# Kernel tuning notes

Measured on AMD Instinct MI355X. Metric: run time of the kernel, lower is better.

## Reference

```python
import jax, jax.numpy as jnp
import numpy as np

N = 50000      # nodes
E = 800000     # edges (avg degree 16)
F = 128        # num_features
H = 128        # hidden_channels
C = 16         # num_classes
KEEP = 0.5     # dropout keep prob


def setup_inputs() -> dict:
    key = jax.random.key(0)
    ks = jax.random.split(key, 7)
    x = jax.random.normal(ks[0], (N, F), dtype=jnp.float32)
    edge_index = jax.random.randint(ks[1], (2, E), 0, N, dtype=jnp.int64)
    W1 = jax.random.normal(ks[2], (F, H), dtype=jnp.float32) / np.float32(np.sqrt(F))
    b1 = jnp.zeros((H,), dtype=jnp.float32)
    W2 = jax.random.normal(ks[3], (H, C), dtype=jnp.float32) / np.float32(np.sqrt(H))
    b2 = jnp.zeros((C,), dtype=jnp.float32)
    # deterministic dropout mask (train-mode dropout, prob=0.5), pre-scaled by 1/keep
    dropout_mask = (jax.random.uniform(ks[4], (N, H)) < KEEP).astype(jnp.float32) / np.float32(KEEP)
    return {"x": x, "edge_index": edge_index, "W1": W1, "b1": b1,
            "W2": W2, "b2": b2, "dropout_mask": dropout_mask}


def _gather_mean(h, src, dst, n_nodes):
    # irregular gather (h[src]) + segment scatter-add at dst, then mean by in-degree
    agg = jax.ops.segment_sum(h[src], dst, num_segments=n_nodes)  # [N, c]
    deg = jax.ops.segment_sum(jnp.ones_like(dst, dtype=h.dtype), dst, num_segments=n_nodes)
    return agg / jnp.maximum(deg, 1.0)[:, None]


def reference(x, edge_index, W1, b1, W2, b2, dropout_mask):
    src, dst = edge_index[0], edge_index[1]
    # linmaps1: 0th->1st order broadcast; identity for singleton reference domains
    h = _gather_mean(x, src, dst, N)          # ConvolutionalLayer_1P #1: gather
    h = h @ W1 + b1                           # linear transform
    h = jax.nn.relu(h)
    h = h * dropout_mask                      # Dropout(prob=0.5)
    h = _gather_mean(h, src, dst, N)          # ConvolutionalLayer_1P #2: gather
    out = h @ W2 + b2
    # linmaps0: 1st->0th order reduce; identity for singleton domains
    return out
```

## Files before the change

### kernel.cpp

```cpp
#include <hip/hip_runtime.h>

#define NNODES 50000
#define NEDGES 800000
#define FDIM 128
#define HDIM 128
#define CDIM 16

#define NBUCK 256
#define BCAP 6144
#define NBA 391
#define NMB 782

typedef __attribute__((ext_vector_type(8))) short bf16x8;
typedef __attribute__((ext_vector_type(4))) float f32x4;

__device__ __forceinline__ ushort f32_to_bf16_rne(float f) {
  unsigned u = __float_as_uint(f);
  unsigned rounded = u + 0x7fffu + ((u >> 16) & 1u);
  return (ushort)(rounded >> 16);
}
__device__ __forceinline__ float bf_lo(unsigned u) { return __uint_as_float(u << 16); }
__device__ __forceinline__ float bf_hi(unsigned u) { return __uint_as_float(u & 0xffff0000u); }

__global__ __launch_bounds__(256) void k_binA(
    const int* __restrict__ src, const int* __restrict__ dst,
    int* __restrict__ gcur, unsigned* __restrict__ ebuf,
    const float* __restrict__ mask, unsigned* __restrict__ maskb) {
  __shared__ int cnt[NBUCK];
  __shared__ int base[NBUCK];
  int tid = threadIdx.x;
  if (blockIdx.x < NBA) {
    int e0 = blockIdx.x * 2048;
    cnt[tid] = 0;
    __syncthreads();
    int sv[8], dv[8];
    #pragma unroll
    for (int i = 0; i < 8; ++i) {
      int e = e0 + i * 256 + tid;
      if (e < NEDGES) {
        sv[i] = src[e];
        dv[i] = dst[e];
        atomicAdd(&cnt[dv[i] >> 8], 1);
      } else {
        dv[i] = -1;
      }
    }
    __syncthreads();
    base[tid] = atomicAdd(&gcur[tid], cnt[tid]);
    cnt[tid] = 0;
    __syncthreads();
    #pragma unroll
    for (int i = 0; i < 8; ++i) {
      if (dv[i] >= 0) {
        int b = dv[i] >> 8;
        int pos = base[b] + atomicAdd(&cnt[b], 1);
        if (pos < BCAP)
          ebuf[b * BCAP + pos] = ((unsigned)(dv[i] & 255) << 16) | (unsigned)sv[i];
      }
    }
    return;
  }
  int t = (blockIdx.x - NBA) * 256 + tid;
  if (t < 200000) {
    const float* mp = mask + (size_t)t * 32;
    unsigned bits = 0;
    #pragma unroll
    for (int i = 0; i < 8; ++i) {
      float4 m = *reinterpret_cast<const float4*>(mp + i * 4);
      bits |= (m.x != 0.f ? 1u : 0u) << (i * 4 + 0);
      bits |= (m.y != 0.f ? 1u : 0u) << (i * 4 + 1);
      bits |= (m.z != 0.f ? 1u : 0u) << (i * 4 + 2);
      bits |= (m.w != 0.f ? 1u : 0u) << (i * 4 + 3);
    }
    maskb[t] = bits;
  }
}

__global__ __launch_bounds__(256) void k_binB_cast(
    const int* __restrict__ gcur, const unsigned* __restrict__ ebuf,
    int* __restrict__ deg, int* __restrict__ offs, ushort* __restrict__ ssrc,
    const float* __restrict__ x, ushort* __restrict__ xh,
    const float* __restrict__ W1, ushort* __restrict__ W1T,
    const float* __restrict__ W2, ushort* __restrict__ W2T) {
  __shared__ int s[NBUCK];
  __shared__ int doff[NBUCK];
  __shared__ int dcur[NBUCK];
  int tid = threadIdx.x;
  if (blockIdx.x < NBUCK) {
    int b = blockIdx.x;
    int c = gcur[tid];
    if (c > BCAP) c = BCAP;
    s[tid] = c;
    for (int off = 1; off < 256; off <<= 1) {
      __syncthreads();
      int t = (tid >= off) ? s[tid - off] : 0;
      __syncthreads();
      s[tid] += t;
    }
    __syncthreads();
    int my_base = (b > 0) ? s[b - 1] : 0;
    int count = s[b] - my_base;

    dcur[tid] = 0;
    __syncthreads();
    const unsigned* eb = &ebuf[b * BCAP];
    for (int e = tid; e < count; e += 256) {
      atomicAdd(&dcur[eb[e] >> 16], 1);
    }
    __syncthreads();
    int dn = dcur[tid];
    s[tid] = dn;
    for (int off = 1; off < 256; off <<= 1) {
      __syncthreads();
      int t = (tid >= off) ? s[tid - off] : 0;
      __syncthreads();
      s[tid] += t;
    }
    __syncthreads();
    doff[tid] = s[tid] - dn;
    int node = b * 256 + tid;
    if (node < NNODES) {
      deg[node] = dn;
      offs[node] = my_base + doff[tid];
    }
    dcur[tid] = 0;
    __syncthreads();

    for (int e = tid; e < count; e += 256) {
      unsigned v = eb[e];
      int loc = v >> 16;
      int pos = my_base + doff[loc] + atomicAdd(&dcur[loc], 1);
      ssrc[pos] = (ushort)(v & 0xffffu);
    }
    return;
  }
  int t = (blockIdx.x - NBUCK) * 256 + tid;
  if (t < 1600000) {
    float4 v = *reinterpret_cast<const float4*>(&x[t * 4]);
    ushort4 o;
    o.x = f32_to_bf16_rne(v.x);
    o.y = f32_to_bf16_rne(v.y);
    o.z = f32_to_bf16_rne(v.z);
    o.w = f32_to_bf16_rne(v.w);
    *reinterpret_cast<ushort4*>(&xh[t * 4]) = o;
    return;
  }
  t -= 1600000;
  if (t < 16384) {
    int c = t >> 7, k = t & 127;
    W1T[c * 128 + k] = f32_to_bf16_rne(W1[k * 128 + c]);
    return;
  }
  t -= 16384;
  if (t < 2048) {
    int c = t >> 7, k = t & 127;
    W2T[c * 128 + k] = f32_to_bf16_rne(W2[k * 16 + c]);
  }
}

__global__ __launch_bounds__(256) void k_spmm1(
    const ushort* __restrict__ xh, const int* __restrict__ offs,
    const int* __restrict__ deg, const ushort* __restrict__ ssrc,
    ushort* __restrict__ aggh) {
  int tid = threadIdx.x;
  int grp = tid >> 4;
  int l16 = tid & 15;
  int n = blockIdx.x * 16 + grp;
  if (n >= NNODES) return;
  int start = offs[n];
  int d = deg[n];
  const ushort* base = xh + l16 * 8;
  float a0[8] = {0,0,0,0,0,0,0,0};
  float a1[8] = {0,0,0,0,0,0,0,0};
  float a2[8] = {0,0,0,0,0,0,0,0};
  float a3[8] = {0,0,0,0,0,0,0,0};
  int j = 0;
  for (; j + 3 < d; j += 4) {
    int s0 = ssrc[start + j + 0];
    int s1 = ssrc[start + j + 1];
    int s2 = ssrc[start + j + 2];
    int s3 = ssrc[start + j + 3];
    uint4 u0 = *reinterpret_cast<const uint4*>(base + s0 * FDIM);
    uint4 u1 = *reinterpret_cast<const uint4*>(base + s1 * FDIM);
    uint4 u2 = *reinterpret_cast<const uint4*>(base + s2 * FDIM);
    uint4 u3 = *reinterpret_cast<const uint4*>(base + s3 * FDIM);
    a0[0] += bf_lo(u0.x); a0[1] += bf_hi(u0.x); a0[2] += bf_lo(u0.y); a0[3] += bf_hi(u0.y);
    a0[4] += bf_lo(u0.z); a0[5] += bf_hi(u0.z); a0[6] += bf_lo(u0.w); a0[7] += bf_hi(u0.w);
    a1[0] += bf_lo(u1.x); a1[1] += bf_hi(u1.x); a1[2] += bf_lo(u1.y); a1[3] += bf_hi(u1.y);
    a1[4] += bf_lo(u1.z); a1[5] += bf_hi(u1.z); a1[6] += bf_lo(u1.w); a1[7] += bf_hi(u1.w);
    a2[0] += bf_lo(u2.x); a2[1] += bf_hi(u2.x); a2[2] += bf_lo(u2.y); a2[3] += bf_hi(u2.y);
    a2[4] += bf_lo(u2.z); a2[5] += bf_hi(u2.z); a2[6] += bf_lo(u2.w); a2[7] += bf_hi(u2.w);
    a3[0] += bf_lo(u3.x); a3[1] += bf_hi(u3.x); a3[2] += bf_lo(u3.y); a3[3] += bf_hi(u3.y);
    a3[4] += bf_lo(u3.z); a3[5] += bf_hi(u3.z); a3[6] += bf_lo(u3.w); a3[7] += bf_hi(u3.w);
  }
  for (; j < d; ++j) {
    int s0 = ssrc[start + j];
    uint4 u0 = *reinterpret_cast<const uint4*>(base + s0 * FDIM);
    a0[0] += bf_lo(u0.x); a0[1] += bf_hi(u0.x); a0[2] += bf_lo(u0.y); a0[3] += bf_hi(u0.y);
    a0[4] += bf_lo(u0.z); a0[5] += bf_hi(u0.z); a0[6] += bf_lo(u0.w); a0[7] += bf_hi(u0.w);
  }
  float inv = 1.0f / (float)(d > 0 ? d : 1);
  unsigned r[4];
  #pragma unroll
  for (int k = 0; k < 4; ++k) {
    float e0 = (a0[2 * k] + a1[2 * k] + a2[2 * k] + a3[2 * k]) * inv;
    float e1 = (a0[2 * k + 1] + a1[2 * k + 1] + a2[2 * k + 1] + a3[2 * k + 1]) * inv;
    r[k] = (unsigned)f32_to_bf16_rne(e0) | ((unsigned)f32_to_bf16_rne(e1) << 16);
  }
  uint4 o; o.x = r[0]; o.y = r[1]; o.z = r[2]; o.w = r[3];
  *reinterpret_cast<uint4*>(&aggh[(size_t)n * FDIM + l16 * 8]) = o;
}

#define HT_STRIDE 132
__global__ __launch_bounds__(256) void k_dense(
    const ushort* __restrict__ aggh, const ushort* __restrict__ W1T,
    const float* __restrict__ b1, const unsigned* __restrict__ maskb,
    const ushort* __restrict__ W2T, ushort* __restrict__ zh) {
  __shared__ ushort hT[4][16 * HT_STRIDE];
  int w = threadIdx.x >> 6;
  int lane = threadIdx.x & 63;
  int nw = blockIdx.x * 64 + w * 16;
  if (nw >= NNODES) return;
  int l15 = lane & 15, quad = lane >> 4;

  f32x4 acc[8];
  #pragma unroll
  for (int ct = 0; ct < 8; ++ct) acc[ct] = (f32x4){0.f, 0.f, 0.f, 0.f};

  uint4 mb[4];
  #pragma unroll
  for (int r = 0; r < 4; ++r) {
    mb[r] = *reinterpret_cast<const uint4*>(&maskb[(size_t)(nw + quad * 4 + r) * 4]);
  }

  const ushort* arow = &aggh[(size_t)(nw + l15) * 128 + quad * 8];
  #pragma unroll
  for (int kk = 0; kk < 4; ++kk) {
    bf16x8 a = *reinterpret_cast<const bf16x8*>(arow + kk * 32);
    #pragma unroll
    for (int ct = 0; ct < 8; ++ct) {
      bf16x8 b = *reinterpret_cast<const bf16x8*>(
          &W1T[(size_t)(ct * 16 + l15) * 128 + kk * 32 + quad * 8]);
      acc[ct] = __builtin_amdgcn_mfma_f32_16x16x32_bf16(a, b, acc[ct], 0, 0, 0);
    }
  }

  ushort* ht = hT[w];
  #pragma unroll
  for (int ct = 0; ct < 8; ++ct) {
    int col = ct * 16 + l15;
    float bb = b1[col];
    int shift = (ct & 1) * 16 + l15;
    #pragma unroll
    for (int r = 0; r < 4; ++r) {
      unsigned word = (ct & 2) ? ((ct & 4) ? mb[r].w : mb[r].y)
                               : ((ct & 4) ? mb[r].z : mb[r].x);
      float v = acc[ct][r] + bb;
      v = v > 0.f ? v : 0.f;
      v = ((word >> shift) & 1u) ? (v + v) : 0.f;
      ht[(quad * 4 + r) * HT_STRIDE + col] = f32_to_bf16_rne(v);
    }
  }

  f32x4 zacc = (f32x4){0.f, 0.f, 0.f, 0.f};
  #pragma unroll
  for (int kk = 0; kk < 4; ++kk) {
    const ushort* ap = &ht[l15 * HT_STRIDE + kk * 32 + quad * 8];
    ushort4 alo = *reinterpret_cast<const ushort4*>(ap);
    ushort4 ahi = *reinterpret_cast<const ushort4*>(ap + 4);
    bf16x8 a2 = (bf16x8){(short)alo.x, (short)alo.y, (short)alo.z, (short)alo.w,
                         (short)ahi.x, (short)ahi.y, (short)ahi.z, (short)ahi.w};
    bf16x8 b2 = *reinterpret_cast<const bf16x8*>(&W2T[l15 * 128 + kk * 32 + quad * 8]);
    zacc = __builtin_amdgcn_mfma_f32_16x16x32_bf16(a2, b2, zacc, 0, 0, 0);
  }
  #pragma unroll
  for (int r = 0; r < 4; ++r) {
    zh[(size_t)(nw + quad * 4 + r) * 16 + l15] = f32_to_bf16_rne(zacc[r]);
  }
}

__global__ __launch_bounds__(256) void k_spmm2(
    const ushort* __restrict__ zh, const int* __restrict__ offs,
    const int* __restrict__ deg, const ushort* __restrict__ ssrc,
    const float* __restrict__ b2, float* __restrict__ out) {
  int tid = threadIdx.x;
  int nl = tid >> 3, c2 = tid & 7;
  int n = blockIdx.x * 32 + nl;
  if (n >= NNODES) return;
  int start = offs[n], d = deg[n];
  const ushort* zb = zh + c2 * 2;
  float a0 = 0.f, a1 = 0.f, b0 = 0.f, b1v = 0.f;
  float c0 = 0.f, c1 = 0.f, d0 = 0.f, d1 = 0.f;
  int j = 0;
  for (; j + 7 < d; j += 8) {
    int s0 = ssrc[start + j + 0], s1 = ssrc[start + j + 1];
    int s2 = ssrc[start + j + 2], s3 = ssrc[start + j + 3];
    int s4 = ssrc[start + j + 4], s5 = ssrc[start + j + 5];
    int s6 = ssrc[start + j + 6], s7 = ssrc[start + j + 7];
    unsigned u0 = *reinterpret_cast<const unsigned*>(zb + s0 * 16);
    unsigned u1 = *reinterpret_cast<const unsigned*>(zb + s1 * 16);
    unsigned u2 = *reinterpret_cast<const unsigned*>(zb + s2 * 16);
    unsigned u3 = *reinterpret_cast<const unsigned*>(zb + s3 * 16);
    unsigned u4 = *reinterpret_cast<const unsigned*>(zb + s4 * 16);
    unsigned u5 = *reinterpret_cast<const unsigned*>(zb + s5 * 16);
    unsigned u6 = *reinterpret_cast<const unsigned*>(zb + s6 * 16);
    unsigned u7 = *reinterpret_cast<const unsigned*>(zb + s7 * 16);
    a0 += bf_lo(u0); a1 += bf_hi(u0);
    b0 += bf_lo(u1); b1v += bf_hi(u1);
    c0 += bf_lo(u2); c1 += bf_hi(u2);
    d0 += bf_lo(u3); d1 += bf_hi(u3);
    a0 += bf_lo(u4); a1 += bf_hi(u4);
    b0 += bf_lo(u5); b1v += bf_hi(u5);
    c0 += bf_lo(u6); c1 += bf_hi(u6);
    d0 += bf_lo(u7); d1 += bf_hi(u7);
  }
  for (; j < d; ++j) {
    int s0 = ssrc[start + j];
    unsigned u0 = *reinterpret_cast<const unsigned*>(zb + s0 * 16);
    a0 += bf_lo(u0); a1 += bf_hi(u0);
  }
  float inv = 1.0f / (float)(d > 0 ? d : 1);
  float o0 = ((a0 + b0) + (c0 + d0)) * inv + b2[c2 * 2 + 0];
  float o1 = ((a1 + b1v) + (c1 + d1)) * inv + b2[c2 * 2 + 1];
  float2 o; o.x = o0; o.y = o1;
  *reinterpret_cast<float2*>(&out[(size_t)n * 16 + c2 * 2]) = o;
}


extern "C" void kernel_launch(void* const* d_in, const int* in_sizes, int n_in,
                              void* d_out, int out_size, void* d_ws, size_t ws_size,
                              hipStream_t stream) {
  const float* x    = (const float*)d_in[0];
  const int*   ei   = (const int*)d_in[1];
  const float* W1   = (const float*)d_in[2];
  const float* b1   = (const float*)d_in[3];
  const float* W2   = (const float*)d_in[4];
  const float* b2   = (const float*)d_in[5];
  const float* mask = (const float*)d_in[6];
  float* out = (float*)d_out;

  const int* src = ei;
  const int* dst = ei + NEDGES;

  char* ws = (char*)d_ws;
  size_t o = 0;
  auto alloc = [&](size_t bytes) -> void* {
    void* p = ws + o;
    o += (bytes + 255) & ~(size_t)255;
    return p;
  };
  ushort*   aggh  = (ushort*)alloc((size_t)NNODES * 128 * 2);
  ushort*   xh    = (ushort*)alloc((size_t)NNODES * 128 * 2);
  ushort*   zh    = (ushort*)alloc((size_t)NNODES * 16 * 2);
  ushort*   W1T   = (ushort*)alloc((size_t)128 * 128 * 2);
  ushort*   W2T   = (ushort*)alloc((size_t)16 * 128 * 2);
  int*      deg   = (int*)alloc((size_t)NNODES * 4);
  int*      offs  = (int*)alloc((size_t)NNODES * 4);
  int*      gcur  = (int*)alloc((size_t)NBUCK * 4);
  unsigned* ebuf  = (unsigned*)alloc((size_t)NBUCK * BCAP * 4);
  ushort*   ssrc  = (ushort*)alloc((size_t)NEDGES * 2);
  unsigned* maskb = (unsigned*)alloc((size_t)NNODES * 4 * 4);

  int cast_blocks = (1600000 + 16384 + 2048 + 255) / 256;

  hipMemsetAsync(gcur, 0, NBUCK * sizeof(int), stream);
  k_binA<<<NBA + NMB, 256, 0, stream>>>(src, dst, gcur, ebuf, mask, maskb);
  k_binB_cast<<<NBUCK + cast_blocks, 256, 0, stream>>>(gcur, ebuf, deg, offs, ssrc,
                                                       x, xh, W1, W1T, W2, W2T);
  k_spmm1<<<(NNODES + 15) / 16, 256, 0, stream>>>(xh, offs, deg, ssrc, aggh);
  k_dense<<<(NNODES + 63) / 64, 256, 0, stream>>>(aggh, W1T, b1, maskb, W2T, zh);
  k_spmm2<<<(NNODES + 31) / 32, 256, 0, stream>>>(zh, offs, deg, ssrc, b2, out);
}
```

Before: 181.8 us.

## Fuse first neighbor gather into dense MFMA kernel, dropping aggregated intermediate

Merges the first SpMM gather with the dense MLP kernel. Each lane gathers the neighbor rows directly into its MFMA A-fragment layout (node per lane m, 32-element k-slices per quad) and feeds them straight to the W1 MFMAs. This removes the aggh write and re-read and one kernel launch. The cost is that each lane now walks its own node's edge list serially with four 16-byte loads per edge, so lanes with different degrees diverge. The work is also spread over fewer threads, which reduces memory-level parallelism compared with the old 16-lanes-per-node gather.

```diff
diff --git a/kernel.cpp b/kernel.cpp
--- a/kernel.cpp
+++ b/kernel.cpp
@@ -158,99 +158,100 @@
   }
 }
 
-__global__ __launch_bounds__(256) void k_spmm1(
+#define ACCQ(A, U) do { \
+    A[0] += bf_lo(U.x); A[1] += bf_hi(U.x); \
+    A[2] += bf_lo(U.y); A[3] += bf_hi(U.y); \
+    A[4] += bf_lo(U.z); A[5] += bf_hi(U.z); \
+    A[6] += bf_lo(U.w); A[7] += bf_hi(U.w); } while (0)
+
+#define HT_STRIDE 132
+__global__ __launch_bounds__(256) void k_gather_dense(
     const ushort* __restrict__ xh, const int* __restrict__ offs,
     const int* __restrict__ deg, const ushort* __restrict__ ssrc,
-    ushort* __restrict__ aggh) {
-  int tid = threadIdx.x;
-  int grp = tid >> 4;
-  int l16 = tid & 15;
-  int n = blockIdx.x * 16 + grp;
-  if (n >= NNODES) return;
-  int start = offs[n];
-  int d = deg[n];
-  const ushort* base = xh + l16 * 8;
+    const ushort* __restrict__ W1T, const float* __restrict__ b1,
+    const unsigned* __restrict__ maskb, const ushort* __restrict__ W2T,
+    ushort* __restrict__ zh) {
+  __shared__ ushort hT[4][16 * HT_STRIDE];
+  int w = threadIdx.x >> 6;
+  int lane = threadIdx.x & 63;
+  int m = lane & 15, quad = lane >> 4;
+  int nw = blockIdx.x * 64 + w * 16;
+  int n = nw + m;
+  int start = 0, d = 0;
+  if (n < NNODES) { start = offs[n]; d = deg[n]; }
+
   float a0[8] = {0,0,0,0,0,0,0,0};
   float a1[8] = {0,0,0,0,0,0,0,0};
   float a2[8] = {0,0,0,0,0,0,0,0};
   float a3[8] = {0,0,0,0,0,0,0,0};
+  const ushort* xb = xh + quad * 8;
   int j = 0;
-  for (; j + 3 < d; j += 4) {
-    int s0 = ssrc[start + j + 0];
+  for (; j + 1 < d; j += 2) {
+    int s0 = ssrc[start + j];
     int s1 = ssrc[start + j + 1];
-    int s2 = ssrc[start + j + 2];
-    int s3 = ssrc[start + j + 3];
-    uint4 u0 = *reinterpret_cast<const uint4*>(base + s0 * FDIM);
-    uint4 u1 = *reinterpret_cast<const uint4*>(base + s1 * FDIM);
-    uint4 u2 = *reinterpret_cast<const uint4*>(base + s2 * FDIM);
-    uint4 u3 = *reinterpret_cast<const uint4*>(base + s3 * FDIM);
-    a0[0] += bf_lo(u0.x); a0[1] += bf_hi(u0.x); a0[2] += bf_lo(u0.y); a0[3] += bf_hi(u0.y);
-    a0[4] += bf_lo(u0.z); a0[5] += bf_hi(u0.z); a0[6] += bf_lo(u0.w); a0[7] += bf_hi(u0.w);
-    a1[0] += bf_lo(u1.x); a1[1] += bf_hi(u1.x); a1[2] += bf_lo(u1.y); a1[3] += bf_hi(u1.y);
-    a1[4] += bf_lo(u1.z); a1[5] += bf_hi(u1.z); a1[6] += bf_lo(u1.w); a1[7] += bf_hi(u1.w);
-    a2[0] += bf_lo(u2.x); a2[1] += bf_hi(u2.x); a2[2] += bf_lo(u2.y); a2[3] += bf_hi(u2.y);
-    a2[4] += bf_lo(u2.z); a2[5] += bf_hi(u2.z); a2[6] += bf_lo(u2.w); a2[7] += bf_hi(u2.w);
-    a3[0] += bf_lo(u3.x); a3[1] += bf_hi(u3.x); a3[2] += bf_lo(u3.y); a3[3] += bf_hi(u3.y);
-    a3[4] += bf_lo(u3.z); a3[5] += bf_hi(u3.z); a3[6] += bf_lo(u3.w); a3[7] += bf_hi(u3.w);
-  }
-  for (; j < d; ++j) {
+    const ushort* r0 = xb + s0 * FDIM;
+    const ushort* r1 = xb + s1 * FDIM;
+    uint4 u00 = *reinterpret_cast<const uint4*>(r0);
+    uint4 u01 = *reinterpret_cast<const uint4*>(r0 + 32);
+    uint4 u02 = *reinterpret_cast<const uint4*>(r0 + 64);
+    uint4 u03 = *reinterpret_cast<const uint4*>(r0 + 96);
+    uint4 u10 = *reinterpret_cast<const uint4*>(r1);
+    uint4 u11 = *reinterpret_cast<const uint4*>(r1 + 32);
+    uint4 u12 = *reinterpret_cast<const uint4*>(r1 + 64);
+    uint4 u13 = *reinterpret_cast<const uint4*>(r1 + 96);
+    ACCQ(a0, u00); ACCQ(a1, u01); ACCQ(a2, u02); ACCQ(a3, u03);
+    ACCQ(a0, u10); ACCQ(a1, u11); ACCQ(a2, u12); ACCQ(a3, u13);
+  }
+  if (j < d) {
     int s0 = ssrc[start + j];
-    uint4 u0 = *reinterpret_cast<const uint4*>(base + s0 * FDIM);
-    a0[0] += bf_lo(u0.x); a0[1] += bf_hi(u0.x); a0[2] += bf_lo(u0.y); a0[3] += bf_hi(u0.y);
-    a0[4] += bf_lo(u0.z); a0[5] += bf_hi(u0.z); a0[6] += bf_lo(u0.w); a0[7] += bf_hi(u0.w);
+    const ushort* r0 = xb + s0 * FDIM;
+    uint4 u00 = *reinterpret_cast<const uint4*>(r0);
+    uint4 u01 = *reinterpret_cast<const uint4*>(r0 + 32);
+    uint4 u02 = *reinterpret_cast<const uint4*>(r0 + 64);
+    uint4 u03 = *reinterpret_cast<const uint4*>(r0 + 96);
+    ACCQ(a0, u00); ACCQ(a1, u01); ACCQ(a2, u02); ACCQ(a3, u03);
   }
   float inv = 1.0f / (float)(d > 0 ? d : 1);
-  unsigned r[4];
-  #pragma unroll
-  for (int k = 0; k < 4; ++k) {
-    float e0 = (a0[2 * k] + a1[2 * k] + a2[2 * k] + a3[2 * k]) * inv;
-    float e1 = (a0[2 * k + 1] + a1[2 * k + 1] + a2[2 * k + 1] + a3[2 * k + 1]) * inv;
-    r[k] = (unsigned)f32_to_bf16_rne(e0) | ((unsigned)f32_to_bf16_rne(e1) << 16);
-  }
-  uint4 o; o.x = r[0]; o.y = r[1]; o.z = r[2]; o.w = r[3];
-  *reinterpret_cast<uint4*>(&aggh[(size_t)n * FDIM + l16 * 8]) = o;
-}
-
-#define HT_STRIDE 132
-__global__ __launch_bounds__(256) void k_dense(
-    const ushort* __restrict__ aggh, const ushort* __restrict__ W1T,
-    const float* __restrict__ b1, const unsigned* __restrict__ maskb,
-    const ushort* __restrict__ W2T, ushort* __restrict__ zh) {
-  __shared__ ushort hT[4][16 * HT_STRIDE];
-  int w = threadIdx.x >> 6;
-  int lane = threadIdx.x & 63;
-  int nw = blockIdx.x * 64 + w * 16;
-  if (nw >= NNODES) return;
-  int l15 = lane & 15, quad = lane >> 4;
+  #define PACK8(A) (bf16x8){ \
+      (short)f32_to_bf16_rne(A[0] * inv), (short)f32_to_bf16_rne(A[1] * inv), \
+      (short)f32_to_bf16_rne(A[2] * inv), (short)f32_to_bf16_rne(A[3] * inv), \
+      (short)f32_to_bf16_rne(A[4] * inv), (short)f32_to_bf16_rne(A[5] * inv), \
+      (short)f32_to_bf16_rne(A[6] * inv), (short)f32_to_bf16_rne(A[7] * inv)}
+  bf16x8 af0 = PACK8(a0);
+  bf16x8 af1 = PACK8(a1);
+  bf16x8 af2 = PACK8(a2);
+  bf16x8 af3 = PACK8(a3);
 
   f32x4 acc[8];
   #pragma unroll
   for (int ct = 0; ct < 8; ++ct) acc[ct] = (f32x4){0.f, 0.f, 0.f, 0.f};
+  #pragma unroll
+  for (int ct = 0; ct < 8; ++ct) {
+    const ushort* bp = &W1T[(size_t)(ct * 16 + m) * 128 + quad * 8];
+    acc[ct] = __builtin_amdgcn_mfma_f32_16x16x32_bf16(
+        af0, *reinterpret_cast<const bf16x8*>(bp), acc[ct], 0, 0, 0);
+    acc[ct] = __builtin_amdgcn_mfma_f32_16x16x32_bf16(
+        af1, *reinterpret_cast<const bf16x8*>(bp + 32), acc[ct], 0, 0, 0);
+    acc[ct] = __builtin_amdgcn_mfma_f32_16x16x32_bf16(
+        af2, *reinterpret_cast<const bf16x8*>(bp + 64), acc[ct], 0, 0, 0);
+    acc[ct] = __builtin_amdgcn_mfma_f32_16x16x32_bf16(
+        af3, *reinterpret_cast<const bf16x8*>(bp + 96), acc[ct], 0, 0, 0);
+  }
 
   uint4 mb[4];
   #pragma unroll
   for (int r = 0; r < 4; ++r) {
-    mb[r] = *reinterpret_cast<const uint4*>(&maskb[(size_t)(nw + quad * 4 + r) * 4]);
-  }
-
-  const ushort* arow = &aggh[(size_t)(nw + l15) * 128 + quad * 8];
-  #pragma unroll
-  for (int kk = 0; kk < 4; ++kk) {
-    bf16x8 a = *reinterpret_cast<const bf16x8*>(arow + kk * 32);
-    #pragma unroll
-    for (int ct = 0; ct < 8; ++ct) {
-      bf16x8 b = *reinterpret_cast<const bf16x8*>(
-          &W1T[(size_t)(ct * 16 + l15) * 128 + kk * 32 + quad * 8]);
-      acc[ct] = __builtin_amdgcn_mfma_f32_16x16x32_bf16(a, b, acc[ct], 0, 0, 0);
-    }
+    int nr = nw + quad * 4 + r;
+    if (nr >= NNODES) nr = NNODES - 1;
+    mb[r] = *reinterpret_cast<const uint4*>(&maskb[(size_t)nr * 4]);
   }
 
   ushort* ht = hT[w];
   #pragma unroll
   for (int ct = 0; ct < 8; ++ct) {
-    int col = ct * 16 + l15;
+    int col = ct * 16 + m;
     float bb = b1[col];
-    int shift = (ct & 1) * 16 + l15;
+    int shift = (ct & 1) * 16 + m;
     #pragma unroll
     for (int r = 0; r < 4; ++r) {
       unsigned word = (ct & 2) ? ((ct & 4) ? mb[r].w : mb[r].y)
@@ -265,17 +266,19 @@
   f32x4 zacc = (f32x4){0.f, 0.f, 0.f, 0.f};
   #pragma unroll
   for (int kk = 0; kk < 4; ++kk) {
-    const ushort* ap = &ht[l15 * HT_STRIDE + kk * 32 + quad * 8];
+    const ushort* ap = &ht[m * HT_STRIDE + kk * 32 + quad * 8];
     ushort4 alo = *reinterpret_cast<const ushort4*>(ap);
     ushort4 ahi = *reinterpret_cast<const ushort4*>(ap + 4);
-    bf16x8 a2 = (bf16x8){(short)alo.x, (short)alo.y, (short)alo.z, (short)alo.w,
-                         (short)ahi.x, (short)ahi.y, (short)ahi.z, (short)ahi.w};
-    bf16x8 b2 = *reinterpret_cast<const bf16x8*>(&W2T[l15 * 128 + kk * 32 + quad * 8]);
-    zacc = __builtin_amdgcn_mfma_f32_16x16x32_bf16(a2, b2, zacc, 0, 0, 0);
+    bf16x8 afr = (bf16x8){(short)alo.x, (short)alo.y, (short)alo.z, (short)alo.w,
+                          (short)ahi.x, (short)ahi.y, (short)ahi.z, (short)ahi.w};
+    bf16x8 b2 = *reinterpret_cast<const bf16x8*>(&W2T[m * 128 + kk * 32 + quad * 8]);
+    zacc = __builtin_amdgcn_mfma_f32_16x16x32_bf16(afr, b2, zacc, 0, 0, 0);
   }
   #pragma unroll
   for (int r = 0; r < 4; ++r) {
-    zh[(size_t)(nw + quad * 4 + r) * 16 + l15] = f32_to_bf16_rne(zacc[r]);
+    int node = nw + quad * 4 + r;
+    if (node < NNODES)
+      zh[(size_t)node * 16 + m] = f32_to_bf16_rne(zacc[r]);
   }
 }
 
@@ -349,7 +352,6 @@
     o += (bytes + 255) & ~(size_t)255;
     return p;
   };
-  ushort*   aggh  = (ushort*)alloc((size_t)NNODES * 128 * 2);
   ushort*   xh    = (ushort*)alloc((size_t)NNODES * 128 * 2);
   ushort*   zh    = (ushort*)alloc((size_t)NNODES * 16 * 2);
   ushort*   W1T   = (ushort*)alloc((size_t)128 * 128 * 2);
@@ -367,7 +369,7 @@
   k_binA<<<NBA + NMB, 256, 0, stream>>>(src, dst, gcur, ebuf, mask, maskb);
   k_binB_cast<<<NBUCK + cast_blocks, 256, 0, stream>>>(gcur, ebuf, deg, offs, ssrc,
                                                        x, xh, W1, W1T, W2, W2T);
-  k_spmm1<<<(NNODES + 15) / 16, 256, 0, stream>>>(xh, offs, deg, ssrc, aggh);
-  k_dense<<<(NNODES + 63) / 64, 256, 0, stream>>>(aggh, W1T, b1, maskb, W2T, zh);
+  k_gather_dense<<<(NNODES + 63) / 64, 256, 0, stream>>>(xh, offs, deg, ssrc,
+                                                         W1T, b1, maskb, W2T, zh);
   k_spmm2<<<(NNODES + 31) / 32, 256, 0, stream>>>(zh, offs, deg, ssrc, b2, out);
 }
```

Measured after the change: 188.6 us. 3.7% more time.

## Fuse first gather-mean SpMM with dense W1/ReLU/dropout/W2 stage via shared memory

Applied to the files above, without the earlier changes.

Merges the first neighbor aggregation kernel with the dense MLP kernel. Each block aggregates 16 nodes into shared memory, then splits the W1 MFMA output tiles across its four waves before one wave runs the W2 projection. This removes the aggh global round trip (a write and reread of N×128 bf16) and one kernel launch. In exchange it adds two block barriers, leaves three waves idle during the W2 step, and drops the bounds check, which relies on N being divisible by 16.

```diff
diff --git a/kernel.cpp b/kernel.cpp
--- a/kernel.cpp
+++ b/kernel.cpp
@@ -158,15 +158,20 @@
   }
 }
 
-__global__ __launch_bounds__(256) void k_spmm1(
+#define HT_STRIDE 132
+__global__ __launch_bounds__(256) void k_fused1(
     const ushort* __restrict__ xh, const int* __restrict__ offs,
     const int* __restrict__ deg, const ushort* __restrict__ ssrc,
-    ushort* __restrict__ aggh) {
+    const ushort* __restrict__ W1T, const float* __restrict__ b1,
+    const unsigned* __restrict__ maskb, const ushort* __restrict__ W2T,
+    ushort* __restrict__ zh) {
+  __shared__ ushort sh[16 * HT_STRIDE];
+  __shared__ ushort ht[16 * HT_STRIDE];
   int tid = threadIdx.x;
   int grp = tid >> 4;
   int l16 = tid & 15;
-  int n = blockIdx.x * 16 + grp;
-  if (n >= NNODES) return;
+  int nw = blockIdx.x * 16;
+  int n = nw + grp;
   int start = offs[n];
   int d = deg[n];
   const ushort* base = xh + l16 * 8;
@@ -207,75 +212,74 @@
     float e1 = (a0[2 * k + 1] + a1[2 * k + 1] + a2[2 * k + 1] + a3[2 * k + 1]) * inv;
     r[k] = (unsigned)f32_to_bf16_rne(e0) | ((unsigned)f32_to_bf16_rne(e1) << 16);
   }
-  uint4 o; o.x = r[0]; o.y = r[1]; o.z = r[2]; o.w = r[3];
-  *reinterpret_cast<uint4*>(&aggh[(size_t)n * FDIM + l16 * 8]) = o;
-}
-
-#define HT_STRIDE 132
-__global__ __launch_bounds__(256) void k_dense(
-    const ushort* __restrict__ aggh, const ushort* __restrict__ W1T,
-    const float* __restrict__ b1, const unsigned* __restrict__ maskb,
-    const ushort* __restrict__ W2T, ushort* __restrict__ zh) {
-  __shared__ ushort hT[4][16 * HT_STRIDE];
-  int w = threadIdx.x >> 6;
-  int lane = threadIdx.x & 63;
-  int nw = blockIdx.x * 64 + w * 16;
-  if (nw >= NNODES) return;
-  int l15 = lane & 15, quad = lane >> 4;
-
-  f32x4 acc[8];
-  #pragma unroll
-  for (int ct = 0; ct < 8; ++ct) acc[ct] = (f32x4){0.f, 0.f, 0.f, 0.f};
-
-  uint4 mb[4];
-  #pragma unroll
-  for (int r = 0; r < 4; ++r) {
-    mb[r] = *reinterpret_cast<const uint4*>(&maskb[(size_t)(nw + quad * 4 + r) * 4]);
-  }
-
-  const ushort* arow = &aggh[(size_t)(nw + l15) * 128 + quad * 8];
+  *reinterpret_cast<uint4*>(&sh[grp * HT_STRIDE + l16 * 8]) =
+      (uint4){r[0], r[1], r[2], r[3]};
+  __syncthreads();
+
+  int w = tid >> 6;
+  int lane = tid & 63;
+  int m = lane & 15, quad = lane >> 4;
+  int ct0 = 2 * w, ct1 = 2 * w + 1;
+
+  bf16x8 af[4];
   #pragma unroll
   for (int kk = 0; kk < 4; ++kk) {
-    bf16x8 a = *reinterpret_cast<const bf16x8*>(arow + kk * 32);
-    #pragma unroll
-    for (int ct = 0; ct < 8; ++ct) {
-      bf16x8 b = *reinterpret_cast<const bf16x8*>(
-          &W1T[(size_t)(ct * 16 + l15) * 128 + kk * 32 + quad * 8]);
-      acc[ct] = __builtin_amdgcn_mfma_f32_16x16x32_bf16(a, b, acc[ct], 0, 0, 0);
-    }
-  }
-
-  ushort* ht = hT[w];
-  #pragma unroll
-  for (int ct = 0; ct < 8; ++ct) {
-    int col = ct * 16 + l15;
-    float bb = b1[col];
-    int shift = (ct & 1) * 16 + l15;
-    #pragma unroll
-    for (int r = 0; r < 4; ++r) {
-      unsigned word = (ct & 2) ? ((ct & 4) ? mb[r].w : mb[r].y)
-                               : ((ct & 4) ? mb[r].z : mb[r].x);
-      float v = acc[ct][r] + bb;
-      v = v > 0.f ? v : 0.f;
-      v = ((word >> shift) & 1u) ? (v + v) : 0.f;
-      ht[(quad * 4 + r) * HT_STRIDE + col] = f32_to_bf16_rne(v);
-    }
-  }
-
-  f32x4 zacc = (f32x4){0.f, 0.f, 0.f, 0.f};
-  #pragma unroll
-  for (int kk = 0; kk < 4; ++kk) {
-    const ushort* ap = &ht[l15 * HT_STRIDE + kk * 32 + quad * 8];
+    const ushort* ap = &sh[m * HT_STRIDE + kk * 32 + quad * 8];
     ushort4 alo = *reinterpret_cast<const ushort4*>(ap);
     ushort4 ahi = *reinterpret_cast<const ushort4*>(ap + 4);
-    bf16x8 a2 = (bf16x8){(short)alo.x, (short)alo.y, (short)alo.z, (short)alo.w,
-                         (short)ahi.x, (short)ahi.y, (short)ahi.z, (short)ahi.w};
-    bf16x8 b2 = *reinterpret_cast<const bf16x8*>(&W2T[l15 * 128 + kk * 32 + quad * 8]);
-    zacc = __builtin_amdgcn_mfma_f32_16x16x32_bf16(a2, b2, zacc, 0, 0, 0);
-  }
-  #pragma unroll
-  for (int r = 0; r < 4; ++r) {
-    zh[(size_t)(nw + quad * 4 + r) * 16 + l15] = f32_to_bf16_rne(zacc[r]);
+    af[kk] = (bf16x8){(short)alo.x, (short)alo.y, (short)alo.z, (short)alo.w,
+                      (short)ahi.x, (short)ahi.y, (short)ahi.z, (short)ahi.w};
+  }
+  f32x4 acc0 = (f32x4){0.f, 0.f, 0.f, 0.f};
+  f32x4 acc1 = (f32x4){0.f, 0.f, 0.f, 0.f};
+  const ushort* bp0 = &W1T[(size_t)(ct0 * 16 + m) * 128 + quad * 8];
+  const ushort* bp1 = &W1T[(size_t)(ct1 * 16 + m) * 128 + quad * 8];
+  #pragma unroll
+  for (int kk = 0; kk < 4; ++kk) {
+    acc0 = __builtin_amdgcn_mfma_f32_16x16x32_bf16(
+        af[kk], *reinterpret_cast<const bf16x8*>(bp0 + kk * 32), acc0, 0, 0, 0);
+    acc1 = __builtin_amdgcn_mfma_f32_16x16x32_bf16(
+        af[kk], *reinterpret_cast<const bf16x8*>(bp1 + kk * 32), acc1, 0, 0, 0);
+  }
+
+  unsigned mbw[4];
+  #pragma unroll
+  for (int rr = 0; rr < 4; ++rr) {
+    mbw[rr] = maskb[(size_t)(nw + quad * 4 + rr) * 4 + w];
+  }
+  float bb0 = b1[ct0 * 16 + m];
+  float bb1 = b1[ct1 * 16 + m];
+  int sh0 = m;
+  int sh1 = 16 + m;
+  #pragma unroll
+  for (int rr = 0; rr < 4; ++rr) {
+    float v0 = acc0[rr] + bb0;
+    v0 = v0 > 0.f ? v0 : 0.f;
+    v0 = ((mbw[rr] >> sh0) & 1u) ? (v0 + v0) : 0.f;
+    ht[(quad * 4 + rr) * HT_STRIDE + ct0 * 16 + m] = f32_to_bf16_rne(v0);
+    float v1 = acc1[rr] + bb1;
+    v1 = v1 > 0.f ? v1 : 0.f;
+    v1 = ((mbw[rr] >> sh1) & 1u) ? (v1 + v1) : 0.f;
+    ht[(quad * 4 + rr) * HT_STRIDE + ct1 * 16 + m] = f32_to_bf16_rne(v1);
+  }
+  __syncthreads();
+
+  if (w == 0) {
+    f32x4 zacc = (f32x4){0.f, 0.f, 0.f, 0.f};
+    #pragma unroll
+    for (int kk = 0; kk < 4; ++kk) {
+      const ushort* ap = &ht[m * HT_STRIDE + kk * 32 + quad * 8];
+      ushort4 alo = *reinterpret_cast<const ushort4*>(ap);
+      ushort4 ahi = *reinterpret_cast<const ushort4*>(ap + 4);
+      bf16x8 afr = (bf16x8){(short)alo.x, (short)alo.y, (short)alo.z, (short)alo.w,
+                            (short)ahi.x, (short)ahi.y, (short)ahi.z, (short)ahi.w};
+      bf16x8 b2f = *reinterpret_cast<const bf16x8*>(&W2T[m * 128 + kk * 32 + quad * 8]);
+      zacc = __builtin_amdgcn_mfma_f32_16x16x32_bf16(afr, b2f, zacc, 0, 0, 0);
+    }
+    #pragma unroll
+    for (int rr = 0; rr < 4; ++rr) {
+      zh[(size_t)(nw + quad * 4 + rr) * 16 + m] = f32_to_bf16_rne(zacc[rr]);
+    }
   }
 }
 
@@ -349,7 +353,6 @@
     o += (bytes + 255) & ~(size_t)255;
     return p;
   };
-  ushort*   aggh  = (ushort*)alloc((size_t)NNODES * 128 * 2);
   ushort*   xh    = (ushort*)alloc((size_t)NNODES * 128 * 2);
   ushort*   zh    = (ushort*)alloc((size_t)NNODES * 16 * 2);
   ushort*   W1T   = (ushort*)alloc((size_t)128 * 128 * 2);
@@ -367,7 +370,7 @@
   k_binA<<<NBA + NMB, 256, 0, stream>>>(src, dst, gcur, ebuf, mask, maskb);
   k_binB_cast<<<NBUCK + cast_blocks, 256, 0, stream>>>(gcur, ebuf, deg, offs, ssrc,
                                                        x, xh, W1, W1T, W2, W2T);
-  k_spmm1<<<(NNODES + 15) / 16, 256, 0, stream>>>(xh, offs, deg, ssrc, aggh);
-  k_dense<<<(NNODES + 63) / 64, 256, 0, stream>>>(aggh, W1T, b1, maskb, W2T, zh);
+  k_fused1<<<NNODES / 16, 256, 0, stream>>>(xh, offs, deg, ssrc,
+                                            W1T, b1, maskb, W2T, zh);
   k_spmm2<<<(NNODES + 31) / 32, 256, 0, stream>>>(zh, offs, deg, ssrc, b2, out);
 }
```

New measurement: 172.2 us (median of 2 runs). 1.06x faster.

## Split xh into column quarters and map quarters to XCD pairs in spmm1

Applied to the files above, without the earlier changes.

The bf16 copy of x is stored as four column-quarter planes of 32 features each, and the first gather kernel assigns each quarter to a pair of XCDs through the block index. Each XCD's L2 then only has to hold a 3.2 MB slice of the feature table instead of the whole 12.8 MB table, which should raise gather cache hit rates. Each node's quarter is handled by 4 lanes with an 8-way unrolled loop and a single accumulator, and the output is written with nontemporal stores. The scheme relies on blocks being dispatched round-robin across 8 XCDs, and with only four lanes per row each row fetch is 64 bytes, so access granularity gets finer.

```diff
diff --git a/kernel.cpp b/kernel.cpp
--- a/kernel.cpp
+++ b/kernel.cpp
@@ -10,9 +10,12 @@
 #define BCAP 6144
 #define NBA 391
 #define NMB 782
+#define NQ 4
+#define NT1 782
 
 typedef __attribute__((ext_vector_type(8))) short bf16x8;
 typedef __attribute__((ext_vector_type(4))) float f32x4;
+typedef __attribute__((ext_vector_type(4))) unsigned u32x4;
 
 __device__ __forceinline__ ushort f32_to_bf16_rne(float f) {
   unsigned u = __float_as_uint(f);
@@ -142,7 +145,11 @@
     o.y = f32_to_bf16_rne(v.y);
     o.z = f32_to_bf16_rne(v.z);
     o.w = f32_to_bf16_rne(v.w);
-    *reinterpret_cast<ushort4*>(&xh[t * 4]) = o;
+    int e0 = t * 4;
+    int n = e0 >> 7;
+    int c = e0 & 127;
+    int idx = ((c >> 5) * NNODES + n) * 32 + (c & 31);
+    *reinterpret_cast<ushort4*>(&xh[idx]) = o;
     return;
   }
   t -= 1600000;
@@ -158,57 +165,64 @@
   }
 }
 
-__global__ __launch_bounds__(256) void k_spmm1(
+#define ACCA(A, U) do { \
+    A[0] += bf_lo(U.x); A[1] += bf_hi(U.x); \
+    A[2] += bf_lo(U.y); A[3] += bf_hi(U.y); \
+    A[4] += bf_lo(U.z); A[5] += bf_hi(U.z); \
+    A[6] += bf_lo(U.w); A[7] += bf_hi(U.w); } while (0)
+
+__global__ __launch_bounds__(256) void k_spmm1x(
     const ushort* __restrict__ xh, const int* __restrict__ offs,
     const int* __restrict__ deg, const ushort* __restrict__ ssrc,
     ushort* __restrict__ aggh) {
+  int b = blockIdx.x;
+  int xcd = b & 7;
+  int q = xcd >> 1;
+  int nb = (b >> 3) * 2 + (xcd & 1);
   int tid = threadIdx.x;
-  int grp = tid >> 4;
-  int l16 = tid & 15;
-  int n = blockIdx.x * 16 + grp;
+  int grp = tid >> 2;
+  int l4 = tid & 3;
+  int n = nb * 64 + grp;
   if (n >= NNODES) return;
   int start = offs[n];
   int d = deg[n];
-  const ushort* base = xh + l16 * 8;
-  float a0[8] = {0,0,0,0,0,0,0,0};
-  float a1[8] = {0,0,0,0,0,0,0,0};
-  float a2[8] = {0,0,0,0,0,0,0,0};
-  float a3[8] = {0,0,0,0,0,0,0,0};
+  const ushort* xq = xh + (size_t)q * NNODES * 32 + l4 * 8;
+  float acc[8] = {0, 0, 0, 0, 0, 0, 0, 0};
   int j = 0;
-  for (; j + 3 < d; j += 4) {
+  for (; j + 7 < d; j += 8) {
     int s0 = ssrc[start + j + 0];
     int s1 = ssrc[start + j + 1];
     int s2 = ssrc[start + j + 2];
     int s3 = ssrc[start + j + 3];
-    uint4 u0 = *reinterpret_cast<const uint4*>(base + s0 * FDIM);
-    uint4 u1 = *reinterpret_cast<const uint4*>(base + s1 * FDIM);
-    uint4 u2 = *reinterpret_cast<const uint4*>(base + s2 * FDIM);
-    uint4 u3 = *reinterpret_cast<const uint4*>(base + s3 * FDIM);
-    a0[0] += bf_lo(u0.x); a0[1] += bf_hi(u0.x); a0[2] += bf_lo(u0.y); a0[3] += bf_hi(u0.y);
-    a0[4] += bf_lo(u0.z); a0[5] += bf_hi(u0.z); a0[6] += bf_lo(u0.w); a0[7] += bf_hi(u0.w);
-    a1[0] += bf_lo(u1.x); a1[1] += bf_hi(u1.x); a1[2] += bf_lo(u1.y); a1[3] += bf_hi(u1.y);
-    a1[4] += bf_lo(u1.z); a1[5] += bf_hi(u1.z); a1[6] += bf_lo(u1.w); a1[7] += bf_hi(u1.w);
-    a2[0] += bf_lo(u2.x); a2[1] += bf_hi(u2.x); a2[2] += bf_lo(u2.y); a2[3] += bf_hi(u2.y);
-    a2[4] += bf_lo(u2.z); a2[5] += bf_hi(u2.z); a2[6] += bf_lo(u2.w); a2[7] += bf_hi(u2.w);
-    a3[0] += bf_lo(u3.x); a3[1] += bf_hi(u3.x); a3[2] += bf_lo(u3.y); a3[3] += bf_hi(u3.y);
-    a3[4] += bf_lo(u3.z); a3[5] += bf_hi(u3.z); a3[6] += bf_lo(u3.w); a3[7] += bf_hi(u3.w);
+    int s4 = ssrc[start + j + 4];
+    int s5 = ssrc[start + j + 5];
+    int s6 = ssrc[start + j + 6];
+    int s7 = ssrc[start + j + 7];
+    uint4 u0 = *reinterpret_cast<const uint4*>(xq + ((size_t)s0 << 5));
+    uint4 u1 = *reinterpret_cast<const uint4*>(xq + ((size_t)s1 << 5));
+    uint4 u2 = *reinterpret_cast<const uint4*>(xq + ((size_t)s2 << 5));
+    uint4 u3 = *reinterpret_cast<const uint4*>(xq + ((size_t)s3 << 5));
+    uint4 u4 = *reinterpret_cast<const uint4*>(xq + ((size_t)s4 << 5));
+    uint4 u5 = *reinterpret_cast<const uint4*>(xq + ((size_t)s5 << 5));
+    uint4 u6 = *reinterpret_cast<const uint4*>(xq + ((size_t)s6 << 5));
+    uint4 u7 = *reinterpret_cast<const uint4*>(xq + ((size_t)s7 << 5));
+    ACCA(acc, u0); ACCA(acc, u1); ACCA(acc, u2); ACCA(acc, u3);
+    ACCA(acc, u4); ACCA(acc, u5); ACCA(acc, u6); ACCA(acc, u7);
   }
   for (; j < d; ++j) {
     int s0 = ssrc[start + j];
-    uint4 u0 = *reinterpret_cast<const uint4*>(base + s0 * FDIM);
-    a0[0] += bf_lo(u0.x); a0[1] += bf_hi(u0.x); a0[2] += bf_lo(u0.y); a0[3] += bf_hi(u0.y);
-    a0[4] += bf_lo(u0.z); a0[5] += bf_hi(u0.z); a0[6] += bf_lo(u0.w); a0[7] += bf_hi(u0.w);
+    uint4 u0 = *reinterpret_cast<const uint4*>(xq + ((size_t)s0 << 5));
+    ACCA(acc, u0);
   }
   float inv = 1.0f / (float)(d > 0 ? d : 1);
-  unsigned r[4];
+  u32x4 o;
   #pragma unroll
   for (int k = 0; k < 4; ++k) {
-    float e0 = (a0[2 * k] + a1[2 * k] + a2[2 * k] + a3[2 * k]) * inv;
-    float e1 = (a0[2 * k + 1] + a1[2 * k + 1] + a2[2 * k + 1] + a3[2 * k + 1]) * inv;
-    r[k] = (unsigned)f32_to_bf16_rne(e0) | ((unsigned)f32_to_bf16_rne(e1) << 16);
-  }
-  uint4 o; o.x = r[0]; o.y = r[1]; o.z = r[2]; o.w = r[3];
-  *reinterpret_cast<uint4*>(&aggh[(size_t)n * FDIM + l16 * 8]) = o;
+    o[k] = (unsigned)f32_to_bf16_rne(acc[2 * k] * inv) |
+           ((unsigned)f32_to_bf16_rne(acc[2 * k + 1] * inv) << 16);
+  }
+  __builtin_nontemporal_store(
+      o, reinterpret_cast<u32x4*>(&aggh[(size_t)n * 128 + q * 32 + l4 * 8]));
 }
 
 #define HT_STRIDE 132
@@ -349,8 +363,8 @@
     o += (bytes + 255) & ~(size_t)255;
     return p;
   };
+  ushort*   xh    = (ushort*)alloc((size_t)NNODES * 128 * 2);
   ushort*   aggh  = (ushort*)alloc((size_t)NNODES * 128 * 2);
-  ushort*   xh    = (ushort*)alloc((size_t)NNODES * 128 * 2);
   ushort*   zh    = (ushort*)alloc((size_t)NNODES * 16 * 2);
   ushort*   W1T   = (ushort*)alloc((size_t)128 * 128 * 2);
   ushort*   W2T   = (ushort*)alloc((size_t)16 * 128 * 2);
@@ -367,7 +381,7 @@
   k_binA<<<NBA + NMB, 256, 0, stream>>>(src, dst, gcur, ebuf, mask, maskb);
   k_binB_cast<<<NBUCK + cast_blocks, 256, 0, stream>>>(gcur, ebuf, deg, offs, ssrc,
                                                        x, xh, W1, W1T, W2, W2T);
-  k_spmm1<<<(NNODES + 15) / 16, 256, 0, stream>>>(xh, offs, deg, ssrc, aggh);
+  k_spmm1x<<<NT1 / 2 * 8, 256, 0, stream>>>(xh, offs, deg, ssrc, aggh);
   k_dense<<<(NNODES + 63) / 64, 256, 0, stream>>>(aggh, W1T, b1, maskb, W2T, zh);
   k_spmm2<<<(NNODES + 31) / 32, 256, 0, stream>>>(zh, offs, deg, ssrc, b2, out);
 }
```

Measured after the change: 178.2 us. -2.0%, faster.
